# Kernel tuning notes

Measured on AMD Instinct MI355X. Metric: run time of the kernel, lower is better.

Reference implementation:

```python
import jax, jax.numpy as jnp
import numpy as np

N_NODES = 50000
N_EDGES = 800000
D_IN = 128
D_HID = 128
D_OUT = 128
EPS = 0.1  # GINConv eps


def setup_inputs() -> dict:
    key = jax.random.key(0)
    k = jax.random.split(key, 8)
    scale = 1.0 / np.sqrt(D_IN)
    return {
        "x": jax.random.normal(k[0], (N_NODES, D_IN), dtype=jnp.float32),
        "edge_index": jax.random.randint(k[1], (2, N_EDGES), 0, N_NODES, dtype=jnp.int64),
        "edge_weight": jax.random.uniform(k[2], (N_EDGES,), dtype=jnp.float32),
        "W1a": jax.random.normal(k[3], (D_IN, D_HID), dtype=jnp.float32) * scale,
        "W1b": jax.random.normal(k[4], (D_HID, D_HID), dtype=jnpp.float32) if False else jax.random.normal(k[4], (D_HID, D_HID), dtype=jnp.float32) * scale,
        "W2a": jax.random.normal(k[5], (D_HID, D_HID), dtype=jnp.float32) * scale,
        "W2b": jax.random.normal(k[6], (D_HID, D_OUT), dtype=jnp.float32) * scale,
    }


def _gin_conv(h, src, dst, ew, Wa, Wb, n_nodes):
    # edge-weighted neighbor sum: aggr[i] = sum_{(j->i)} w_ji * h[j]
    msg = ew[:, None] * h[src]                       # [E, d]
    aggr = jax.ops.segment_sum(msg, dst, num_segments=n_nodes)  # [N, d]
    z = (1.0 + EPS) * h + aggr                       # GIN update
    # 2-layer bias-free MLP: lin -> relu -> lin
    return jnp.maximum(z @ Wa, 0.0) @ Wb


def reference(x, edge_index, edge_weight, W1a, W1b, W2a, W2b):
    src, dst = edge_index[0], edge_index[1]
    n = x.shape[0]
    h = _gin_conv(x, src, dst, edge_weight, W1a, W1b, n)
    h = jnp.maximum(h, 0.0)  # relu between convs; dropout is identity in eval
    h = _gin_conv(h, src, dst, edge_weight, W2a, W2b, n)
    return h
```

## Files before the change

kernel.cpp:

```cpp
#include <hip/hip_runtime.h>
#include <hip/hip_fp16.h>

#define D 128
#define N_NODES 50000
#define EPSP1 1.1f

#define NPB 256
#define NBUCK 196
#define CAP 5120
#define P1E 2048

typedef __attribute__((ext_vector_type(8))) short short8;
typedef __attribute__((ext_vector_type(4))) float f32x4;

__device__ __forceinline__ unsigned short f2bf(float f) {
    unsigned u = __float_as_uint(f);
    u += 0x7FFF + ((u >> 16) & 1);
    return (unsigned short)(u >> 16);
}
__device__ __forceinline__ float bf2f(unsigned short h) {
    return __uint_as_float(((unsigned)h) << 16);
}

__global__ __launch_bounds__(256) void fused_pre(
    const int* __restrict__ src, const int* __restrict__ dst,
    const float* __restrict__ ew, int* __restrict__ gcnt,
    uint2* __restrict__ gstage, int ne,
    const float* __restrict__ x, unsigned short* __restrict__ hb, int n4,
    const float* __restrict__ W1a, const float* __restrict__ W1b,
    const float* __restrict__ W2a, const float* __restrict__ W2b,
    unsigned short* __restrict__ wp, int p1grid, int cgrid)
{
    int bid = blockIdx.x;
    int tid = threadIdx.x;
    if (bid < p1grid) {
        __shared__ int bcnt[NBUCK];
        __shared__ int goff[NBUCK];
        if (tid < NBUCK) bcnt[tid] = 0;
        __syncthreads();
        int e0 = bid * P1E;
        int   rank[8];
        int   buck[8];
        uint2 pay[8];
#pragma unroll
        for (int j = 0; j < 8; ++j) {
            int e = e0 + j * 256 + tid;
            buck[j] = -1;
            if (e < ne) {
                int d_ = dst[e];
                int b  = d_ >> 8;
                int dl = d_ & 255;
                pay[j].x = (unsigned)(src[e] & 0xFFFF) | ((unsigned)dl << 16);
                pay[j].y = (unsigned)__half_as_ushort(__float2half_rn(ew[e]));
                rank[j]  = atomicAdd(&bcnt[b], 1);
                buck[j]  = b;
            }
        }
        __syncthreads();
        if (tid < NBUCK && bcnt[tid] > 0)
            goff[tid] = atomicAdd(&gcnt[tid], bcnt[tid]);
        __syncthreads();
#pragma unroll
        for (int j = 0; j < 8; ++j) {
            if (buck[j] >= 0) {
                int pos = goff[buck[j]] + rank[j];
                if (pos < CAP)
                    gstage[(size_t)buck[j] * CAP + pos] = pay[j];
            }
        }
    } else if (bid < p1grid + cgrid) {
        int base = (bid - p1grid) * 1024;
#pragma unroll
        for (int it = 0; it < 4; ++it) {
            int i = base + it * 256 + tid;
            if (i < n4) {
                float4 v = ((const float4*)x)[i];
                ushort4 o;
                o.x = f2bf(v.x); o.y = f2bf(v.y); o.z = f2bf(v.z); o.w = f2bf(v.w);
                ((ushort4*)hb)[i] = o;
            }
        }
    } else {
        int pb = bid - p1grid - cgrid;
        int mat = pb >> 3;
        const float* W = (mat == 0) ? W1a : (mat == 1) ? W1b : (mat == 2) ? W2a : W2b;
        unsigned short* Wp = wp + (size_t)mat * 16384;
        int e = (pb & 7) * 256 + tid;
        int col = e & 127;
        int kq  = e >> 7;
        short8 v;
#pragma unroll
        for (int j = 0; j < 8; ++j)
            v[j] = (short)f2bf(W[(size_t)(kq * 8 + j) * 128 + col]);
        ((short8*)Wp)[e] = v;
    }
}

__global__ __launch_bounds__(512) void csr_build(
    const uint2* __restrict__ gstage, const int* __restrict__ gcnt,
    unsigned* __restrict__ epay, int* __restrict__ off)
{
    __shared__ int hist[NPB];
    __shared__ int scan[NPB];
    __shared__ int bscan[NPB];
    __shared__ int loc[NPB];
    __shared__ unsigned csr[CAP];

    int b = blockIdx.x;
    int t = threadIdx.x;
    int cnt = min(gcnt[b], CAP);

    if (t < NPB) hist[t] = 0;
    __syncthreads();

    uint2 ent[CAP / 512];
#pragma unroll
    for (int it = 0; it < CAP / 512; ++it) {
        int i = it * 512 + t;
        if (i < cnt) {
            ent[it] = gstage[(size_t)b * CAP + i];
            atomicAdd(&hist[(ent[it].x >> 16) & 255], 1);
        }
    }
    __syncthreads();

    if (t < NPB) {
        scan[t]  = hist[t];
        bscan[t] = (t < b) ? min(gcnt[t], CAP) : 0;
    }
    __syncthreads();
    for (int dd = 1; dd < NPB; dd <<= 1) {
        int a0 = 0, a1 = 0;
        if (t < NPB && t >= dd) { a0 = scan[t - dd]; a1 = bscan[t - dd]; }
        __syncthreads();
        if (t < NPB && t >= dd) { scan[t] += a0; bscan[t] += a1; }
        __syncthreads();
    }
    int base = bscan[NPB - 1];

    if (t < NPB) {
        int node = (b << 8) + t;
        int excl = scan[t] - hist[t];
        if (node <= N_NODES) off[node] = base + excl;
        loc[t] = excl;
    }
    __syncthreads();

#pragma unroll
    for (int it = 0; it < CAP / 512; ++it) {
        int i = it * 512 + t;
        if (i < cnt) {
            int dl = (ent[it].x >> 16) & 255;
            int p = atomicAdd(&loc[dl], 1);
            csr[p] = (ent[it].x & 0xFFFF) | (ent[it].y << 16);
        }
    }
    __syncthreads();

    for (int i = t; i < cnt; i += 512)
        epay[base + i] = csr[i];
}

__global__ __launch_bounds__(256) void gather_kernel(
    const unsigned short* __restrict__ h, const int* __restrict__ off,
    const unsigned* __restrict__ epay, unsigned short* __restrict__ z, int n_nodes)
{
    int tid = threadIdx.x;
    int node = blockIdx.x * 4 + (tid >> 6);
    if (node >= n_nodes) return;
    int lane = tid & 63;
    int half = lane >> 5;
    int sub  = lane & 31;
    int beg = off[node];
    int end = off[node + 1];
    float4 acc = make_float4(0.f, 0.f, 0.f, 0.f);
    int i = beg;
    for (; i + 4 <= end; i += 4) {
        unsigned p0 = epay[i + half];
        unsigned p1 = epay[i + 2 + half];
        ushort4 v0 = ((const ushort4*)(h + (size_t)(p0 & 0xFFFF) * D))[sub];
        ushort4 v1 = ((const ushort4*)(h + (size_t)(p1 & 0xFFFF) * D))[sub];
        float w0 = __half2float(__ushort_as_half((unsigned short)(p0 >> 16)));
        float w1 = __half2float(__ushort_as_half((unsigned short)(p1 >> 16)));
        acc.x += w0 * bf2f(v0.x) + w1 * bf2f(v1.x);
        acc.y += w0 * bf2f(v0.y) + w1 * bf2f(v1.y);
        acc.z += w0 * bf2f(v0.z) + w1 * bf2f(v1.z);
        acc.w += w0 * bf2f(v0.w) + w1 * bf2f(v1.w);
    }
    if (i + half < end) {
        unsigned p0 = epay[i + half];
        ushort4 v0 = ((const ushort4*)(h + (size_t)(p0 & 0xFFFF) * D))[sub];
        float w0 = __half2float(__ushort_as_half((unsigned short)(p0 >> 16)));
        acc.x += w0 * bf2f(v0.x);
        acc.y += w0 * bf2f(v0.y);
        acc.z += w0 * bf2f(v0.z);
        acc.w += w0 * bf2f(v0.w);
    }
    if (i + 2 + half < end) {
        unsigned p1 = epay[i + 2 + half];
        ushort4 v1 = ((const ushort4*)(h + (size_t)(p1 & 0xFFFF) * D))[sub];
        float w1 = __half2float(__ushort_as_half((unsigned short)(p1 >> 16)));
        acc.x += w1 * bf2f(v1.x);
        acc.y += w1 * bf2f(v1.y);
        acc.z += w1 * bf2f(v1.z);
        acc.w += w1 * bf2f(v1.w);
    }
    acc.x += __shfl(acc.x, sub + 32, 64);
    acc.y += __shfl(acc.y, sub + 32, 64);
    acc.z += __shfl(acc.z, sub + 32, 64);
    acc.w += __shfl(acc.w, sub + 32, 64);
    if (half == 0) {
        ushort4 xv = ((const ushort4*)(h + (size_t)node * D))[sub];
        acc.x += EPSP1 * bf2f(xv.x);
        acc.y += EPSP1 * bf2f(xv.y);
        acc.z += EPSP1 * bf2f(xv.z);
        acc.w += EPSP1 * bf2f(xv.w);
        ushort4 o;
        o.x = f2bf(acc.x); o.y = f2bf(acc.y); o.z = f2bf(acc.z); o.w = f2bf(acc.w);
        ((ushort4*)(z + (size_t)node * D))[sub] = o;
    }
}

#define TS 136
template<int RELU2, int OUT_F32>
__global__ __launch_bounds__(256) void mlp_fused(
    const unsigned short* __restrict__ A,
    const unsigned short* __restrict__ WpA,
    const unsigned short* __restrict__ WpB,
    void* __restrict__ outv, int n)
{
    __shared__ unsigned short t[128 * TS];

    int tid  = threadIdx.x;
    int wave = tid >> 6;
    int lane = tid & 63;
    int quad = lane >> 4;
    int lc   = lane & 15;
    int rbase = blockIdx.x * 128 + wave * 32;
    int rloc  = wave * 32;

    const short8 zero8 = {0, 0, 0, 0, 0, 0, 0, 0};

    short8 a[2][4];
#pragma unroll
    for (int s = 0; s < 2; ++s) {
        int row = rbase + s * 16 + lc;
        const unsigned short* ap = A + (size_t)row * D;
#pragma unroll
        for (int kk = 0; kk < 4; ++kk)
            a[s][kk] = (row < n) ? *(const short8*)(ap + kk * 32 + quad * 8) : zero8;
    }

    f32x4 acc[2][8];
#pragma unroll
    for (int s = 0; s < 2; ++s)
#pragma unroll
        for (int c = 0; c < 8; ++c)
            acc[s][c] = (f32x4){0.f, 0.f, 0.f, 0.f};

#pragma unroll
    for (int cf = 0; cf < 8; ++cf) {
        short8 b[4];
#pragma unroll
        for (int kk = 0; kk < 4; ++kk)
            b[kk] = *(const short8*)(WpA + ((size_t)(kk * 4 + quad) * 128 + cf * 16 + lc) * 8);
#pragma unroll
        for (int kk = 0; kk < 4; ++kk) {
            acc[0][cf] = __builtin_amdgcn_mfma_f32_16x16x32_bf16(a[0][kk], b[kk], acc[0][cf], 0, 0, 0);
            acc[1][cf] = __builtin_amdgcn_mfma_f32_16x16x32_bf16(a[1][kk], b[kk], acc[1][cf], 0, 0, 0);
        }
    }

#pragma unroll
    for (int s = 0; s < 2; ++s)
#pragma unroll
        for (int reg = 0; reg < 4; ++reg) {
            int row = rloc + s * 16 + quad * 4 + reg;
#pragma unroll
            for (int cf = 0; cf < 8; ++cf)
                t[row * TS + cf * 16 + lc] = f2bf(fmaxf(acc[s][cf][reg], 0.f));
        }
    __syncthreads();

#pragma unroll
    for (int s = 0; s < 2; ++s) {
        int row = rloc + s * 16 + lc;
#pragma unroll
        for (int kk = 0; kk < 4; ++kk)
            a[s][kk] = *(const short8*)&t[row * TS + kk * 32 + quad * 8];
    }
#pragma unroll
    for (int s = 0; s < 2; ++s)
#pragma unroll
        for (int c = 0; c < 8; ++c)
            acc[s][c] = (f32x4){0.f, 0.f, 0.f, 0.f};

#pragma unroll
    for (int cf = 0; cf < 8; ++cf) {
        short8 b[4];
#pragma unroll
        for (int kk = 0; kk < 4; ++kk)
            b[kk] = *(const short8*)(WpB + ((size_t)(kk * 4 + quad) * 128 + cf * 16 + lc) * 8);
#pragma unroll
        for (int kk = 0; kk < 4; ++kk) {
            acc[0][cf] = __builtin_amdgcn_mfma_f32_16x16x32_bf16(a[0][kk], b[kk], acc[0][cf], 0, 0, 0);
            acc[1][cf] = __builtin_amdgcn_mfma_f32_16x16x32_bf16(a[1][kk], b[kk], acc[1][cf], 0, 0, 0);
        }
    }

#pragma unroll
    for (int s = 0; s < 2; ++s)
#pragma unroll
        for (int reg = 0; reg < 4; ++reg) {
            int row = rbase + s * 16 + quad * 4 + reg;
            if (row < n) {
#pragma unroll
                for (int cf = 0; cf < 8; ++cf) {
                    float v = acc[s][cf][reg];
                    if (RELU2) v = fmaxf(v, 0.f);
                    int col = cf * 16 + lc;
                    if (OUT_F32)
                        ((float*)outv)[(size_t)row * D + col] = v;
                    else
                        ((unsigned short*)outv)[(size_t)row * D + col] = f2bf(v);
                }
            }
        }
}

extern "C" void kernel_launch(void* const* d_in, const int* in_sizes, int n_in,
                              void* d_out, int out_size, void* d_ws, size_t ws_size,
                              hipStream_t stream) {
    const float* x   = (const float*)d_in[0];
    const int*   ei  = (const int*)d_in[1];
    const float* ew  = (const float*)d_in[2];
    const float* W1a = (const float*)d_in[3];
    const float* W1b = (const float*)d_in[4];
    const float* W2a = (const float*)d_in[5];
    const float* W2b = (const float*)d_in[6];
    float* out = (float*)d_out;

    int n_edges = in_sizes[2];
    const int* src = ei;
    const int* dst = ei + n_edges;

    size_t node_elems = (size_t)N_NODES * D;
    unsigned short* hb = (unsigned short*)d_ws;
    unsigned short* zb = hb + node_elems;
    unsigned short* wp = zb + node_elems;
    unsigned* epay = (unsigned*)(wp + 4 * 16384);
    uint2*  gstage = (uint2*)(epay + n_edges);
    int*    gcnt   = (int*)(gstage + (size_t)NBUCK * CAP);
    int*    off    = gcnt + NBUCK;

    int p1grid = (n_edges + P1E - 1) / P1E;
    int cgrid  = ((int)(node_elems / 4) + 1023) / 1024;
    int ggrid  = (N_NODES + 127) / 128;
    int agrid  = (N_NODES + 3) / 4;

    hipMemsetAsync(gcnt, 0, NBUCK * sizeof(int), stream);

    fused_pre<<<p1grid + cgrid + 32, 256, 0, stream>>>(
        src, dst, ew, gcnt, gstage, n_edges,
        x, hb, (int)(node_elems / 4),
        W1a, W1b, W2a, W2b, wp, p1grid, cgrid);

    csr_build<<<NBUCK, 512, 0, stream>>>(gstage, gcnt, epay, off);

    unsigned short* wp0 = wp;
    unsigned short* wp1 = wp + 16384;
    unsigned short* wp2 = wp + 2 * 16384;
    unsigned short* wp3 = wp + 3 * 16384;

    gather_kernel<<<agrid, 256, 0, stream>>>(hb, off, epay, zb, N_NODES);
    mlp_fused<1, 0><<<ggrid, 256, 0, stream>>>(zb, wp0, wp1, hb, N_NODES);

    gather_kernel<<<agrid, 256, 0, stream>>>(hb, off, epay, zb, N_NODES);
    mlp_fused<0, 1><<<ggrid, 256, 0, stream>>>(zb, wp2, wp3, out, N_NODES);
}
```

Measured before the change: 213.9 us.

## Fuse neighbor gather into MLP kernel via shared-memory z tile

Merges the gather kernel into the MLP kernel: each wave aggregates its 32 nodes sequentially and writes bf16 z rows into the shared tile, which then feeds the MFMA stage directly. This removes the z round-trip through global memory and two launches, and uses a second buffer so layer 2 reads h2 while layer 1 writes it. The cost is far less parallelism in the gather phase: a grid of about 391 blocks, each wave walking 32 nodes serially, versus 12500 blocks before. That hurts latency hiding on the random gathers. The inner loop is also unrolled to 8 edges to add memory-level parallelism.

```diff
diff --git a/kernel.cpp b/kernel.cpp
--- a/kernel.cpp
+++ b/kernel.cpp
@@ -9,6 +9,7 @@
 #define NBUCK 196
 #define CAP 5120
 #define P1E 2048
+#define TS 136
 
 typedef __attribute__((ext_vector_type(8))) short short8;
 typedef __attribute__((ext_vector_type(4))) float f32x4;
@@ -161,70 +162,10 @@
         epay[base + i] = csr[i];
 }
 
-__global__ __launch_bounds__(256) void gather_kernel(
+template<int RELU2, int OUT_F32>
+__global__ __launch_bounds__(256) void gin_fused(
     const unsigned short* __restrict__ h, const int* __restrict__ off,
-    const unsigned* __restrict__ epay, unsigned short* __restrict__ z, int n_nodes)
-{
-    int tid = threadIdx.x;
-    int node = blockIdx.x * 4 + (tid >> 6);
-    if (node >= n_nodes) return;
-    int lane = tid & 63;
-    int half = lane >> 5;
-    int sub  = lane & 31;
-    int beg = off[node];
-    int end = off[node + 1];
-    float4 acc = make_float4(0.f, 0.f, 0.f, 0.f);
-    int i = beg;
-    for (; i + 4 <= end; i += 4) {
-        unsigned p0 = epay[i + half];
-        unsigned p1 = epay[i + 2 + half];
-        ushort4 v0 = ((const ushort4*)(h + (size_t)(p0 & 0xFFFF) * D))[sub];
-        ushort4 v1 = ((const ushort4*)(h + (size_t)(p1 & 0xFFFF) * D))[sub];
-        float w0 = __half2float(__ushort_as_half((unsigned short)(p0 >> 16)));
-        float w1 = __half2float(__ushort_as_half((unsigned short)(p1 >> 16)));
-        acc.x += w0 * bf2f(v0.x) + w1 * bf2f(v1.x);
-        acc.y += w0 * bf2f(v0.y) + w1 * bf2f(v1.y);
-        acc.z += w0 * bf2f(v0.z) + w1 * bf2f(v1.z);
-        acc.w += w0 * bf2f(v0.w) + w1 * bf2f(v1.w);
-    }
-    if (i + half < end) {
-        unsigned p0 = epay[i + half];
-        ushort4 v0 = ((const ushort4*)(h + (size_t)(p0 & 0xFFFF) * D))[sub];
-        float w0 = __half2float(__ushort_as_half((unsigned short)(p0 >> 16)));
-        acc.x += w0 * bf2f(v0.x);
-        acc.y += w0 * bf2f(v0.y);
-        acc.z += w0 * bf2f(v0.z);
-        acc.w += w0 * bf2f(v0.w);
-    }
-    if (i + 2 + half < end) {
-        unsigned p1 = epay[i + 2 + half];
-        ushort4 v1 = ((const ushort4*)(h + (size_t)(p1 & 0xFFFF) * D))[sub];
-        float w1 = __half2float(__ushort_as_half((unsigned short)(p1 >> 16)));
-        acc.x += w1 * bf2f(v1.x);
-        acc.y += w1 * bf2f(v1.y);
-        acc.z += w1 * bf2f(v1.z);
-        acc.w += w1 * bf2f(v1.w);
-    }
-    acc.x += __shfl(acc.x, sub + 32, 64);
-    acc.y += __shfl(acc.y, sub + 32, 64);
-    acc.z += __shfl(acc.z, sub + 32, 64);
-    acc.w += __shfl(acc.w, sub + 32, 64);
-    if (half == 0) {
-        ushort4 xv = ((const ushort4*)(h + (size_t)node * D))[sub];
-        acc.x += EPSP1 * bf2f(xv.x);
-        acc.y += EPSP1 * bf2f(xv.y);
-        acc.z += EPSP1 * bf2f(xv.z);
-        acc.w += EPSP1 * bf2f(xv.w);
-        ushort4 o;
-        o.x = f2bf(acc.x); o.y = f2bf(acc.y); o.z = f2bf(acc.z); o.w = f2bf(acc.w);
-        ((ushort4*)(z + (size_t)node * D))[sub] = o;
-    }
-}
-
-#define TS 136
-template<int RELU2, int OUT_F32>
-__global__ __launch_bounds__(256) void mlp_fused(
-    const unsigned short* __restrict__ A,
+    const unsigned* __restrict__ epay,
     const unsigned short* __restrict__ WpA,
     const unsigned short* __restrict__ WpB,
     void* __restrict__ outv, int n)
@@ -234,21 +175,76 @@
     int tid  = threadIdx.x;
     int wave = tid >> 6;
     int lane = tid & 63;
+    int half = lane >> 5;
+    int sub  = lane & 31;
     int quad = lane >> 4;
     int lc   = lane & 15;
     int rbase = blockIdx.x * 128 + wave * 32;
     int rloc  = wave * 32;
 
-    const short8 zero8 = {0, 0, 0, 0, 0, 0, 0, 0};
+    for (int j = 0; j < 32; ++j) {
+        int node = rbase + j;
+        float4 acc = make_float4(0.f, 0.f, 0.f, 0.f);
+        if (node < n) {
+            int beg = off[node];
+            int end = off[node + 1];
+            int i = beg;
+            for (; i + 8 <= end; i += 8) {
+                unsigned p0 = epay[i + half];
+                unsigned p1 = epay[i + 2 + half];
+                unsigned p2 = epay[i + 4 + half];
+                unsigned p3 = epay[i + 6 + half];
+                ushort4 v0 = ((const ushort4*)(h + (size_t)(p0 & 0xFFFF) * D))[sub];
+                ushort4 v1 = ((const ushort4*)(h + (size_t)(p1 & 0xFFFF) * D))[sub];
+                ushort4 v2 = ((const ushort4*)(h + (size_t)(p2 & 0xFFFF) * D))[sub];
+                ushort4 v3 = ((const ushort4*)(h + (size_t)(p3 & 0xFFFF) * D))[sub];
+                float w0 = __half2float(__ushort_as_half((unsigned short)(p0 >> 16)));
+                float w1 = __half2float(__ushort_as_half((unsigned short)(p1 >> 16)));
+                float w2 = __half2float(__ushort_as_half((unsigned short)(p2 >> 16)));
+                float w3 = __half2float(__ushort_as_half((unsigned short)(p3 >> 16)));
+                acc.x += w0 * bf2f(v0.x) + w1 * bf2f(v1.x) + w2 * bf2f(v2.x) + w3 * bf2f(v3.x);
+                acc.y += w0 * bf2f(v0.y) + w1 * bf2f(v1.y) + w2 * bf2f(v2.y) + w3 * bf2f(v3.y);
+                acc.z += w0 * bf2f(v0.z) + w1 * bf2f(v1.z) + w2 * bf2f(v2.z) + w3 * bf2f(v3.z);
+                acc.w += w0 * bf2f(v0.w) + w1 * bf2f(v1.w) + w2 * bf2f(v2.w) + w3 * bf2f(v3.w);
+            }
+            for (; i + half < end; i += 2) {
+                unsigned p0 = epay[i + half];
+                ushort4 v0 = ((const ushort4*)(h + (size_t)(p0 & 0xFFFF) * D))[sub];
+                float w0 = __half2float(__ushort_as_half((unsigned short)(p0 >> 16)));
+                acc.x += w0 * bf2f(v0.x);
+                acc.y += w0 * bf2f(v0.y);
+                acc.z += w0 * bf2f(v0.z);
+                acc.w += w0 * bf2f(v0.w);
+            }
+        }
+        acc.x += __shfl(acc.x, sub + 32, 64);
+        acc.y += __shfl(acc.y, sub + 32, 64);
+        acc.z += __shfl(acc.z, sub + 32, 64);
+        acc.w += __shfl(acc.w, sub + 32, 64);
+        if (half == 0) {
+            if (node < n) {
+                ushort4 xv = ((const ushort4*)(h + (size_t)node * D))[sub];
+                acc.x += EPSP1 * bf2f(xv.x);
+                acc.y += EPSP1 * bf2f(xv.y);
+                acc.z += EPSP1 * bf2f(xv.z);
+                acc.w += EPSP1 * bf2f(xv.w);
+            } else {
+                acc = make_float4(0.f, 0.f, 0.f, 0.f);
+            }
+            ushort4 o;
+            o.x = f2bf(acc.x); o.y = f2bf(acc.y); o.z = f2bf(acc.z); o.w = f2bf(acc.w);
+            *(ushort4*)&t[(rloc + j) * TS + sub * 4] = o;
+        }
+    }
+    __syncthreads();
 
     short8 a[2][4];
 #pragma unroll
     for (int s = 0; s < 2; ++s) {
-        int row = rbase + s * 16 + lc;
-        const unsigned short* ap = A + (size_t)row * D;
+        int row = rloc + s * 16 + lc;
 #pragma unroll
         for (int kk = 0; kk < 4; ++kk)
-            a[s][kk] = (row < n) ? *(const short8*)(ap + kk * 32 + quad * 8) : zero8;
+            a[s][kk] = *(const short8*)&t[row * TS + kk * 32 + quad * 8];
     }
 
     f32x4 acc[2][8];
@@ -346,8 +342,8 @@
 
     size_t node_elems = (size_t)N_NODES * D;
     unsigned short* hb = (unsigned short*)d_ws;
-    unsigned short* zb = hb + node_elems;
-    unsigned short* wp = zb + node_elems;
+    unsigned short* h2 = hb + node_elems;
+    unsigned short* wp = h2 + node_elems;
     unsigned* epay = (unsigned*)(wp + 4 * 16384);
     uint2*  gstage = (uint2*)(epay + n_edges);
     int*    gcnt   = (int*)(gstage + (size_t)NBUCK * CAP);
@@ -356,7 +352,6 @@
     int p1grid = (n_edges + P1E - 1) / P1E;
     int cgrid  = ((int)(node_elems / 4) + 1023) / 1024;
     int ggrid  = (N_NODES + 127) / 128;
-    int agrid  = (N_NODES + 3) / 4;
 
     hipMemsetAsync(gcnt, 0, NBUCK * sizeof(int), stream);
 
@@ -372,9 +367,6 @@
     unsigned short* wp2 = wp + 2 * 16384;
     unsigned short* wp3 = wp + 3 * 16384;
 
-    gather_kernel<<<agrid, 256, 0, stream>>>(hb, off, epay, zb, N_NODES);
-    mlp_fused<1, 0><<<ggrid, 256, 0, stream>>>(zb, wp0, wp1, hb, N_NODES);
-
-    gather_kernel<<<agrid, 256, 0, stream>>>(hb, off, epay, zb, N_NODES);
-    mlp_fused<0, 1><<<ggrid, 256, 0, stream>>>(zb, wp2, wp3, out, N_NODES);
-}
+    gin_fused<1, 0><<<ggrid, 256, 0, stream>>>(hb, off, epay, wp0, wp1, h2, N_NODES);
+    gin_fused<0, 1><<<ggrid, 256, 0, stream>>>(h2, off, epay, wp2, wp3, out, N_NODES);
+}
```

Result: slower. 326.0 us (+52.4%).
